# Kernel tuning notes

Measured on AMD Instinct MI355X. Metric: run time of the kernel, lower is better.

Reference implementation:

```python
import jax, jax.numpy as jnp
import numpy as np

B, CIN, COUT, H, W = 64, 64, 64, 32, 32
K, STRIDE, PAD = 3, 1, 1
HOUT = (H + 2 * PAD - K) // STRIDE + 1
WOUT = (W + 2 * PAD - K) // STRIDE + 1


def setup_inputs() -> dict:
    key = jax.random.key(0)
    k1, k2, k3 = jax.random.split(key, 3)
    x = jax.random.normal(k1, (B, CIN, H, W), dtype=jnp.float32)
    # weight: per-location filters (leading singleton batch dim of the torch
    # param is dropped; it only served broadcasting)
    weight = jax.random.normal(k2, (CIN, COUT, HOUT, WOUT, K, K), dtype=jnp.float32)
    bias = jax.random.normal(k3, (COUT, HOUT, WOUT), dtype=jnp.float32)
    return {"x": x, "weight": weight, "bias": bias}


def _extract_patches(x, k, stride, pad, hout, wout):
    # x: [B, C, H, W] -> patches [B, C, k*k, hout, wout]
    xp = jnp.pad(x, ((0, 0), (0, 0), (pad, pad), (pad, pad)))
    slabs = [
        xp[:, :, i : i + (hout - 1) * stride + 1 : stride,
               j : j + (wout - 1) * stride + 1 : stride]
        for i in range(k) for j in range(k)
    ]
    return jnp.stack(slabs, axis=2)


def reference(x, weight, bias):
    cin, cout, hout, wout, k, _ = weight.shape
    patches = _extract_patches(x, k, STRIDE, PAD, hout, wout)  # [B, Cin, k*k, Ho, Wo]
    w = weight.reshape(cin, cout, hout, wout, k * k)
    # fused per-location dot product: avoids the [B,Cin,Cout,Ho,Wo,k,k] intermediate
    y = jnp.einsum('bikhw,iohwk->bohw', patches, w) + bias[None]
    return y
```

## Files before the change

kernel.cpp:

```cpp
#include <hip/hip_runtime.h>
#include <hip/hip_bf16.h>


#define B_    64
#define HW_   32
#define HP_   34
#define NLOC  1024
#define W_OST 9216u
#define W_IST 589824u
#define XT_BYTES  ((size_t)64*HP_*HP_*64*2)
#define WS_NEED   (XT_BYTES)

typedef __attribute__((ext_vector_type(8))) short short8;
typedef __attribute__((ext_vector_type(8))) unsigned short ushort8;
typedef __attribute__((ext_vector_type(4))) float floatx4;

static __device__ __forceinline__ unsigned short f2bf(float f) {
  __hip_bfloat16 h = __float2bfloat16(f);
  return __builtin_bit_cast(unsigned short, h);
}

__global__ __launch_bounds__(256) void xpose_pad(const float* __restrict__ x,
                                                 unsigned short* __restrict__ xt) {
  int bid = blockIdx.x;
  int i = bid / HP_, hh = bid % HP_;
  __shared__ float tile[B_ * 33];
  int t = threadIdx.x;
  bool interior = (hh >= 1 && hh <= HW_);
  if (interior) {
    int h = hh - 1, w = t & 31, bs = t >> 5;
    #pragma unroll
    for (int r = 0; r < 8; ++r) {
      int b = r * 8 + bs;
      tile[b * 33 + w] = x[(((size_t)b * 64 + i) * HW_ + h) * HW_ + w];
    }
  }
  __syncthreads();
  int b = t & 63, wsb = t >> 6;
  size_t base = (size_t)(i * HP_ + hh) * HP_ * B_;
  #pragma unroll
  for (int s = 0; s < 9; ++s) {
    int ww = s * 4 + wsb;
    if (ww < HP_) {
      float v = 0.f;
      if (interior && ww >= 1 && ww <= HW_) v = tile[b * 33 + (ww - 1)];
      xt[base + (size_t)ww * B_ + b] = f2bf(v);
    }
  }
}

__global__ __launch_bounds__(512, 2) void lc2d_fused(
    const unsigned short* __restrict__ xt,
    const float* __restrict__ wsrc,
    const float* __restrict__ bias,
    float* __restrict__ out) {
  __shared__ __align__(16) unsigned short Af[2][4 * 4 * 64 * 8];
  __shared__ __align__(16) unsigned short Bf[2][4 * 4 * 64 * 8];
  __shared__ __align__(16) unsigned short Bs[4 * 2 * 4 * 64 * 8];
  __shared__ __align__(16) unsigned short scr[8][512];

  const int bid  = blockIdx.x;
  const int loc0 = bid << 2;
  const int tid  = threadIdx.x;
  const int lane = tid & 63;
  const int wv8  = tid >> 6;
  const int ll   = wv8 >> 1;
  const int nh   = wv8 & 1;
  const int loc  = loc0 + ll;
  const int hblk = loc >> 5, wblk = loc & 31;
  const int col  = lane & 15;
  const int quad = lane >> 4;
  const int o_0  = nh * 32 + col;

  floatx4 acc[4][2];
  {
    float b0 = bias[(unsigned)o_0 * 1024u + (unsigned)loc];
    float b1 = bias[(unsigned)(o_0 + 16) * 1024u + (unsigned)loc];
    #pragma unroll
    for (int mt = 0; mt < 4; ++mt) {
      acc[mt][0] = (floatx4){b0, b0, b0, b0};
      acc[mt][1] = (floatx4){b1, b1, b1, b1};
    }
  }

  floatx4 wa[5], wb[5];
  const bool lastok = (tid < 256);
  const size_t wrow = (size_t)loc0 * 9;

  auto issueW = [&](int c, floatx4 (&wreg)[5]) {
    const int i0 = c << 2;
    #pragma unroll
    for (int r = 0; r < 5; ++r) {
      if (r < 4 || lastok) {
        int idx = r * 512 + tid;
        int g = idx / 9, p = idx - g * 9;
        int i = i0 + (g >> 6), o = g & 63;
        wreg[r] = *(const floatx4*)(wsrc + (size_t)i * W_IST + (size_t)o * W_OST
                                    + wrow + (size_t)(p * 4));
      }
    }
  };
  auto scatterW = [&](int c, floatx4 (&wreg)[5], unsigned short* bfp) {
    const int i0 = c << 2;
    #pragma unroll
    for (int r = 0; r < 5; ++r) {
      if (r < 4 || lastok) {
        int idx = r * 512 + tid;
        int g = idx / 9, p = idx - g * 9;
        int iq = g >> 6, o = g & 63;
        int ot = o >> 4, oc = o & 15;
        int flane = iq * 16 + oc;
        #pragma unroll
        for (int e = 0; e < 4; ++e) {
          int fi = p * 4 + e;
          int lle = fi / 9, kk = fi - lle * 9;
          unsigned short v = f2bf(wreg[r][e]);
          if (kk < 8) {
            bfp[((lle * 4 + ot) * 64 + flane) * 8 + kk] = v;
          } else {
            int i = i0 + iq;
            int sc = i >> 5, k2 = i & 31;
            Bs[((lle * 8 + sc * 4 + ot) * 64 + (k2 >> 3) * 16 + oc) * 8 + (k2 & 7)] = v;
          }
        }
      }
    }
  };

  auto xtLoad = [&](int t, int s) -> ushort8 {
    int q = (nh << 1) + s;
    int i, kh, kw;
    if (t < 16) {
      i = (t << 2) + q;
      int kk = lane >> 3;
      kh = kk / 3; kw = kk - kh * 3;
    } else {
      i = ((t - 16) << 5) + (q << 3) + (lane >> 3);
      kh = 2; kw = 2;
    }
    return *(const ushort8*)(xt +
        (((unsigned)i * HP_ + (unsigned)(hblk + kh)) * HP_ + (unsigned)(wblk + kw)) * 64u
        + ((unsigned)(lane & 7) << 3));
  };
  auto xposeStore = [&](ushort8 v, int s, unsigned short* afp) {
    const int q = (nh << 1) + s;
    *(ushort8*)&scr[wv8][lane << 3] = v;
    __asm__ volatile("s_waitcnt lgkmcnt(0)" ::: "memory");
    ushort8 p;
    #pragma unroll
    for (int jr = 0; jr < 8; ++jr) p[jr] = scr[wv8][jr * 64 + lane];
    __asm__ volatile("s_waitcnt lgkmcnt(0)" ::: "memory");
    *(ushort8*)(afp + (size_t)((((ll << 2) + (lane >> 4)) << 6)
                               + (q << 4) + (lane & 15)) * 8) = p;
  };

  auto doMFMA = [&](const unsigned short* afp, const unsigned short* bbase, int boff) {
    ushort8 a0 = *(const ushort8*)(afp + (size_t)(((ll << 2) + 0) * 64 + lane) * 8);
    ushort8 a1 = *(const ushort8*)(afp + (size_t)(((ll << 2) + 1) * 64 + lane) * 8);
    ushort8 a2 = *(const ushort8*)(afp + (size_t)(((ll << 2) + 2) * 64 + lane) * 8);
    ushort8 a3 = *(const ushort8*)(afp + (size_t)(((ll << 2) + 3) * 64 + lane) * 8);
    ushort8 b0 = *(const ushort8*)(bbase + (size_t)((boff + 0) * 64 + lane) * 8);
    ushort8 b1 = *(const ushort8*)(bbase + (size_t)((boff + 1) * 64 + lane) * 8);
    acc[0][0] = __builtin_amdgcn_mfma_f32_16x16x32_bf16(
        __builtin_bit_cast(short8, a0), __builtin_bit_cast(short8, b0), acc[0][0], 0, 0, 0);
    acc[1][0] = __builtin_amdgcn_mfma_f32_16x16x32_bf16(
        __builtin_bit_cast(short8, a1), __builtin_bit_cast(short8, b0), acc[1][0], 0, 0, 0);
    acc[2][0] = __builtin_amdgcn_mfma_f32_16x16x32_bf16(
        __builtin_bit_cast(short8, a2), __builtin_bit_cast(short8, b0), acc[2][0], 0, 0, 0);
    acc[3][0] = __builtin_amdgcn_mfma_f32_16x16x32_bf16(
        __builtin_bit_cast(short8, a3), __builtin_bit_cast(short8, b0), acc[3][0], 0, 0, 0);
    acc[0][1] = __builtin_amdgcn_mfma_f32_16x16x32_bf16(
        __builtin_bit_cast(short8, a0), __builtin_bit_cast(short8, b1), acc[0][1], 0, 0, 0);
    acc[1][1] = __builtin_amdgcn_mfma_f32_16x16x32_bf16(
        __builtin_bit_cast(short8, a1), __builtin_bit_cast(short8, b1), acc[1][1], 0, 0, 0);
    acc[2][1] = __builtin_amdgcn_mfma_f32_16x16x32_bf16(
        __builtin_bit_cast(short8, a2), __builtin_bit_cast(short8, b1), acc[2][1], 0, 0, 0);
    acc[3][1] = __builtin_amdgcn_mfma_f32_16x16x32_bf16(
        __builtin_bit_cast(short8, a3), __builtin_bit_cast(short8, b1), acc[3][1], 0, 0, 0);
  };

  issueW(0, wa);
  {
    ushort8 pv0 = xtLoad(0, 0);
    ushort8 pv1 = xtLoad(0, 1);
    xposeStore(pv0, 0, &Af[0][0]);
    xposeStore(pv1, 1, &Af[0][0]);
  }
  scatterW(0, wa, &Bf[0][0]);
  issueW(1, wb);
  __syncthreads();

#define STEP(C, WI, WS) do {                                                  \
    const int c_ = (C);                                                       \
    ushort8 xv0 = xtLoad(c_ + 1, 0);                                          \
    ushort8 xv1 = xtLoad(c_ + 1, 1);                                          \
    if (c_ + 2 <= 15) issueW(c_ + 2, WI);                                     \
    doMFMA(&Af[c_ & 1][0], &Bf[c_ & 1][0], (ll << 2) + (nh << 1));            \
    xposeStore(xv0, 0, &Af[(c_ & 1) ^ 1][0]);                                 \
    xposeStore(xv1, 1, &Af[(c_ & 1) ^ 1][0]);                                 \
    if (c_ + 1 <= 15) scatterW(c_ + 1, WS, &Bf[(c_ & 1) ^ 1][0]);             \
    __syncthreads();                                                          \
  } while (0)

  #pragma unroll 1
  for (int cc = 0; cc < 16; cc += 2) {
    STEP(cc,     wa, wb);
    STEP(cc + 1, wb, wa);
  }
#undef STEP

  {
    ushort8 xv0 = xtLoad(17, 0);
    ushort8 xv1 = xtLoad(17, 1);
    doMFMA(&Af[0][0], &Bs[0], (ll << 3) + 0 + (nh << 1));
    xposeStore(xv0, 0, &Af[1][0]);
    xposeStore(xv1, 1, &Af[1][0]);
    __syncthreads();
    doMFMA(&Af[1][0], &Bs[0], (ll << 3) + 4 + (nh << 1));
  }

  #pragma unroll
  for (int mt = 0; mt < 4; ++mt) {
    int b = mt * 16 + quad * 4;
    #pragma unroll
    for (int r = 0; r < 4; ++r) {
      out[((unsigned)(b + r) * 64u + (unsigned)o_0) * 1024u + (unsigned)loc] = acc[mt][0][r];
      out[((unsigned)(b + r) * 64u + (unsigned)(o_0 + 16)) * 1024u + (unsigned)loc] = acc[mt][1][r];
    }
  }
}

__global__ __launch_bounds__(256, 4) void lc2d_fallback(
    const float* __restrict__ x, const float* __restrict__ weight,
    const float* __restrict__ bias, float* __restrict__ out) {
  int t0 = blockIdx.x;
  int loc = ((t0 & 7) << 7) | (t0 >> 3);
  int h = loc >> 5, w = loc & 31;
  int tid = threadIdx.x;
  int b = tid & 63;
  int o0 = (tid >> 6) * 16;
  __shared__ float As[72 * 64];
  float acc[16];
  #pragma unroll
  for (int j = 0; j < 16; ++j) acc[j] = bias[(size_t)(o0 + j) * NLOC + loc];
  for (int ic = 0; ic < 8; ++ic) {
    __syncthreads();
    #pragma unroll
    for (int s = 0; s < 18; ++s) {
      int f = s * 256 + tid;
      int k = f >> 6, lb = f & 63;
      int kk = k >> 3, isub = k & 7;
      int i = ic * 8 + isub;
      int kh = kk / 3, kw = kk - kh * 3;
      int hh = h + kh - 1, ww = w + kw - 1;
      float v = (hh >= 0 && hh < HW_ && ww >= 0 && ww < HW_)
                  ? x[(((size_t)lb * 64 + i) * HW_ + hh) * HW_ + ww] : 0.f;
      As[k * 64 + lb] = v;
    }
    __syncthreads();
    #pragma unroll 1
    for (int isub = 0; isub < 8; ++isub) {
      const float* wp = weight + (size_t)(ic * 8 + isub) * W_IST
                               + (size_t)o0 * W_OST + loc * 9;
      #pragma unroll
      for (int kk = 0; kk < 9; ++kk) {
        float a = As[(kk * 8 + isub) * 64 + b];
        #pragma unroll
        for (int j = 0; j < 16; ++j)
          acc[j] = fmaf(a, wp[(size_t)j * W_OST + kk], acc[j]);
      }
    }
  }
  size_t ob = ((size_t)b * 64 + o0) * NLOC + loc;
  #pragma unroll
  for (int j = 0; j < 16; ++j) out[ob + (size_t)j * NLOC] = acc[j];
}

extern "C" void kernel_launch(void* const* d_in, const int* in_sizes, int n_in,
                              void* d_out, int out_size, void* d_ws, size_t ws_size,
                              hipStream_t stream) {
  const float* x  = (const float*)d_in[0];
  const float* wt = (const float*)d_in[1];
  const float* bs = (const float*)d_in[2];
  float* out = (float*)d_out;

  if (ws_size >= WS_NEED) {
    unsigned short* xtb = (unsigned short*)d_ws;
    xpose_pad<<<64 * HP_, 256, 0, stream>>>(x, xtb);
    lc2d_fused<<<NLOC / 4, 512, 0, stream>>>(xtb, wt, bs, out);
  } else {
    lc2d_fallback<<<NLOC, 256, 0, stream>>>(x, wt, bs, out);
  }
}
```

Baseline: 263.6 us.

## Split fused kernel across output-channel halves with 256-thread blocks and swizzled block order

Each block now handles 4 locations times 32 output channels (one half) with 4 waves, instead of all 64 output channels with 8 waves. The grid doubles to 512 blocks, and a swizzled block index interleaves the channel halves and locations. Each wave now loads and transposes four input fragments per step, so every block re-gathers the full input patch for its locations. In return it uses half the LDS for weights and gets more blocks for latency hiding. __syncthreads is replaced by a manual lgkmcnt wait plus s_barrier, which skips waiting on outstanding global loads.

```diff
diff --git a/kernel.cpp b/kernel.cpp
--- a/kernel.cpp
+++ b/kernel.cpp
@@ -18,6 +18,11 @@
 static __device__ __forceinline__ unsigned short f2bf(float f) {
   __hip_bfloat16 h = __float2bfloat16(f);
   return __builtin_bit_cast(unsigned short, h);
+}
+
+static __device__ __forceinline__ void soft_barrier() {
+  __asm__ volatile("s_waitcnt lgkmcnt(0)" ::: "memory");
+  __builtin_amdgcn_s_barrier();
 }
 
 __global__ __launch_bounds__(256) void xpose_pad(const float* __restrict__ x,
@@ -49,28 +54,28 @@
   }
 }
 
-__global__ __launch_bounds__(512, 2) void lc2d_fused(
+__global__ __launch_bounds__(256, 2) void lc2d_fused(
     const unsigned short* __restrict__ xt,
     const float* __restrict__ wsrc,
     const float* __restrict__ bias,
     float* __restrict__ out) {
-  __shared__ __align__(16) unsigned short Af[2][4 * 4 * 64 * 8];
-  __shared__ __align__(16) unsigned short Bf[2][4 * 4 * 64 * 8];
-  __shared__ __align__(16) unsigned short Bs[4 * 2 * 4 * 64 * 8];
-  __shared__ __align__(16) unsigned short scr[8][512];
-
-  const int bid  = blockIdx.x;
-  const int loc0 = bid << 2;
-  const int tid  = threadIdx.x;
-  const int lane = tid & 63;
-  const int wv8  = tid >> 6;
-  const int ll   = wv8 >> 1;
-  const int nh   = wv8 & 1;
-  const int loc  = loc0 + ll;
-  const int hblk = loc >> 5, wblk = loc & 31;
-  const int col  = lane & 15;
-  const int quad = lane >> 4;
-  const int o_0  = nh * 32 + col;
+  __shared__ __align__(16) unsigned short Af[2][16 * 64 * 8];
+  __shared__ __align__(16) unsigned short Bf[2][8 * 64 * 8];
+  __shared__ __align__(16) unsigned short Bs[16 * 64 * 8];
+  __shared__ __align__(16) unsigned short scr[4][2][512];
+
+  const int bid   = blockIdx.x;
+  const int lt    = ((bid & 7) << 6) | (bid >> 3);
+  const int ohalf = lt & 1;
+  const int loc0  = (lt >> 1) << 2;
+  const int tid   = threadIdx.x;
+  const int lane  = tid & 63;
+  const int ll    = tid >> 6;
+  const int loc   = loc0 + ll;
+  const int hblk  = loc >> 5, wblk = loc & 31;
+  const int col   = lane & 15;
+  const int quad  = lane >> 4;
+  const int o_0   = ohalf * 32 + col;
 
   floatx4 acc[4][2];
   {
@@ -84,17 +89,18 @@
   }
 
   floatx4 wa[5], wb[5];
-  const bool lastok = (tid < 256);
+  const bool lastok = (tid < 128);
   const size_t wrow = (size_t)loc0 * 9;
+  const unsigned obase = (unsigned)ohalf * 32u;
 
   auto issueW = [&](int c, floatx4 (&wreg)[5]) {
     const int i0 = c << 2;
     #pragma unroll
     for (int r = 0; r < 5; ++r) {
       if (r < 4 || lastok) {
-        int idx = r * 512 + tid;
+        int idx = r * 256 + tid;
         int g = idx / 9, p = idx - g * 9;
-        int i = i0 + (g >> 6), o = g & 63;
+        int i = i0 + (g >> 5), o = (int)obase + (g & 31);
         wreg[r] = *(const floatx4*)(wsrc + (size_t)i * W_IST + (size_t)o * W_OST
                                     + wrow + (size_t)(p * 4));
       }
@@ -105,10 +111,10 @@
     #pragma unroll
     for (int r = 0; r < 5; ++r) {
       if (r < 4 || lastok) {
-        int idx = r * 512 + tid;
+        int idx = r * 256 + tid;
         int g = idx / 9, p = idx - g * 9;
-        int iq = g >> 6, o = g & 63;
-        int ot = o >> 4, oc = o & 15;
+        int iq = g >> 5, ol = g & 31;
+        int ot = ol >> 4, oc = ol & 15;
         int flane = iq * 16 + oc;
         #pragma unroll
         for (int e = 0; e < 4; ++e) {
@@ -116,19 +122,18 @@
           int lle = fi / 9, kk = fi - lle * 9;
           unsigned short v = f2bf(wreg[r][e]);
           if (kk < 8) {
-            bfp[((lle * 4 + ot) * 64 + flane) * 8 + kk] = v;
+            bfp[((lle * 2 + ot) * 64 + flane) * 8 + kk] = v;
           } else {
             int i = i0 + iq;
             int sc = i >> 5, k2 = i & 31;
-            Bs[((lle * 8 + sc * 4 + ot) * 64 + (k2 >> 3) * 16 + oc) * 8 + (k2 & 7)] = v;
+            Bs[(((lle * 2 + sc) * 2 + ot) * 64 + (k2 >> 3) * 16 + oc) * 8 + (k2 & 7)] = v;
           }
         }
       }
     }
   };
 
-  auto xtLoad = [&](int t, int s) -> ushort8 {
-    int q = (nh << 1) + s;
+  auto xtLoad = [&](int t, int q) -> ushort8 {
     int i, kh, kw;
     if (t < 16) {
       i = (t << 2) + q;
@@ -142,16 +147,20 @@
         (((unsigned)i * HP_ + (unsigned)(hblk + kh)) * HP_ + (unsigned)(wblk + kw)) * 64u
         + ((unsigned)(lane & 7) << 3));
   };
-  auto xposeStore = [&](ushort8 v, int s, unsigned short* afp) {
-    const int q = (nh << 1) + s;
-    *(ushort8*)&scr[wv8][lane << 3] = v;
+  auto xposePair = [&](ushort8 v0, ushort8 v1, int q0, unsigned short* afp) {
+    *(ushort8*)&scr[ll][0][lane << 3] = v0;
+    *(ushort8*)&scr[ll][1][lane << 3] = v1;
     __asm__ volatile("s_waitcnt lgkmcnt(0)" ::: "memory");
-    ushort8 p;
-    #pragma unroll
-    for (int jr = 0; jr < 8; ++jr) p[jr] = scr[wv8][jr * 64 + lane];
+    ushort8 p0, p1;
+    #pragma unroll
+    for (int jr = 0; jr < 8; ++jr) p0[jr] = scr[ll][0][jr * 64 + lane];
+    #pragma unroll
+    for (int jr = 0; jr < 8; ++jr) p1[jr] = scr[ll][1][jr * 64 + lane];
     __asm__ volatile("s_waitcnt lgkmcnt(0)" ::: "memory");
     *(ushort8*)(afp + (size_t)((((ll << 2) + (lane >> 4)) << 6)
-                               + (q << 4) + (lane & 15)) * 8) = p;
+                               + (q0 << 4) + (lane & 15)) * 8) = p0;
+    *(ushort8*)(afp + (size_t)((((ll << 2) + (lane >> 4)) << 6)
+                               + ((q0 + 1) << 4) + (lane & 15)) * 8) = p1;
   };
 
   auto doMFMA = [&](const unsigned short* afp, const unsigned short* bbase, int boff) {
@@ -181,25 +190,25 @@
 
   issueW(0, wa);
   {
-    ushort8 pv0 = xtLoad(0, 0);
-    ushort8 pv1 = xtLoad(0, 1);
-    xposeStore(pv0, 0, &Af[0][0]);
-    xposeStore(pv1, 1, &Af[0][0]);
+    ushort8 v0 = xtLoad(0, 0), v1 = xtLoad(0, 1);
+    ushort8 v2 = xtLoad(0, 2), v3 = xtLoad(0, 3);
+    xposePair(v0, v1, 0, &Af[0][0]);
+    xposePair(v2, v3, 2, &Af[0][0]);
   }
   scatterW(0, wa, &Bf[0][0]);
   issueW(1, wb);
-  __syncthreads();
+  soft_barrier();
 
 #define STEP(C, WI, WS) do {                                                  \
     const int c_ = (C);                                                       \
-    ushort8 xv0 = xtLoad(c_ + 1, 0);                                          \
-    ushort8 xv1 = xtLoad(c_ + 1, 1);                                          \
+    ushort8 xv0 = xtLoad(c_ + 1, 0), xv1 = xtLoad(c_ + 1, 1);                 \
+    ushort8 xv2 = xtLoad(c_ + 1, 2), xv3 = xtLoad(c_ + 1, 3);                 \
     if (c_ + 2 <= 15) issueW(c_ + 2, WI);                                     \
-    doMFMA(&Af[c_ & 1][0], &Bf[c_ & 1][0], (ll << 2) + (nh << 1));            \
-    xposeStore(xv0, 0, &Af[(c_ & 1) ^ 1][0]);                                 \
-    xposeStore(xv1, 1, &Af[(c_ & 1) ^ 1][0]);                                 \
+    doMFMA(&Af[c_ & 1][0], &Bf[c_ & 1][0], ll << 1);                          \
+    xposePair(xv0, xv1, 0, &Af[(c_ & 1) ^ 1][0]);                             \
+    xposePair(xv2, xv3, 2, &Af[(c_ & 1) ^ 1][0]);                             \
     if (c_ + 1 <= 15) scatterW(c_ + 1, WS, &Bf[(c_ & 1) ^ 1][0]);             \
-    __syncthreads();                                                          \
+    soft_barrier();                                                           \
   } while (0)
 
   #pragma unroll 1
@@ -210,13 +219,13 @@
 #undef STEP
 
   {
-    ushort8 xv0 = xtLoad(17, 0);
-    ushort8 xv1 = xtLoad(17, 1);
-    doMFMA(&Af[0][0], &Bs[0], (ll << 3) + 0 + (nh << 1));
-    xposeStore(xv0, 0, &Af[1][0]);
-    xposeStore(xv1, 1, &Af[1][0]);
-    __syncthreads();
-    doMFMA(&Af[1][0], &Bs[0], (ll << 3) + 4 + (nh << 1));
+    ushort8 xv0 = xtLoad(17, 0), xv1 = xtLoad(17, 1);
+    ushort8 xv2 = xtLoad(17, 2), xv3 = xtLoad(17, 3);
+    doMFMA(&Af[0][0], &Bs[0], (ll << 1) << 1);
+    xposePair(xv0, xv1, 0, &Af[1][0]);
+    xposePair(xv2, xv3, 2, &Af[1][0]);
+    soft_barrier();
+    doMFMA(&Af[1][0], &Bs[0], ((ll << 1) + 1) << 1);
   }
 
   #pragma unroll
@@ -287,7 +296,7 @@
   if (ws_size >= WS_NEED) {
     unsigned short* xtb = (unsigned short*)d_ws;
     xpose_pad<<<64 * HP_, 256, 0, stream>>>(x, xtb);
-    lc2d_fused<<<NLOC / 4, 512, 0, stream>>>(xtb, wt, bs, out);
+    lc2d_fused<<<512, 256, 0, stream>>>(xtb, wt, bs, out);
   } else {
     lc2d_fallback<<<NLOC, 256, 0, stream>>>(x, wt, bs, out);
   }
```

Result: faster. 252.2 us (-4.3%).
